# Kernel tuning notes

Measured on AMD Instinct MI355X. Metric: run time of the kernel, lower is better.

## Reference

```python
import jax, jax.numpy as jnp
import numpy as np

B, D, DFF, E, TOPK = 16384, 512, 2048, 8, 2


def setup_inputs() -> dict:
    key = jax.random.key(0)
    ks = jax.random.split(key, 5)
    scale_g = 1.0 / np.sqrt(D)
    scale_1 = 1.0 / np.sqrt(D)
    scale_2 = 1.0 / np.sqrt(DFF)
    return {
        "x": jax.random.normal(ks[0], (B, D), dtype=jnp.float32),
        "Wg": jax.random.normal(ks[1], (D, E), dtype=jnp.float32) * scale_g,
        "W1": jax.random.normal(ks[2], (E, D, DFF), dtype=jnp.float32) * scale_1,
        "b1": jnp.zeros((E, DFF), dtype=jnp.float32),
        "W2": jax.random.normal(ks[3], (E, DFF, D), dtype=jnp.float32) * scale_2,
        "b2": jnp.zeros((E, D), dtype=jnp.float32),
    }


def reference(x, Wg, W1, b1, W2, b2):
    # --- gate: top-k softmax routing weights, zeros elsewhere ---
    logits = x @ Wg                              # [B, E]
    probs = jax.nn.softmax(logits, axis=-1)      # [B, E]
    vals, idx = jax.lax.top_k(probs, TOPK)       # [B, K], [B, K]
    routing = jnp.zeros_like(probs).at[jnp.arange(x.shape[0])[:, None], idx].set(vals)  # [B, E]

    # --- experts: dense FFN per expert (equivalent math to masked dispatch) ---
    # original: gather selected tokens per expert, compute, scatter into
    # zeros[E, B, D], multiply by routing.T[:, :, None], sum over experts.
    # routing weight is exactly 0 for unselected tokens, so the dense form
    # out = sum_e routing[b, e] * expert_e(x_b) computes identical results.
    h = jax.nn.relu(jnp.einsum('bd,edf->ebf', x, W1) + b1[:, None, :])  # [E, B, DFF]
    y = jnp.einsum('ebf,efd->ebd', h, W2) + b2[:, None, :]              # [E, B, D]
    out = jnp.einsum('ebd,be->bd', y, routing)                          # [B, D]
    return out
```

## Files before the change

### kernel.cpp

```cpp
#include <hip/hip_runtime.h>
#include <stdint.h>

#define BTOK 16384
#define DM   512
#define DFF  2048
#define NE   8
#define NPAIR (BTOK*2)
#define MAXT 288

typedef short s16x8 __attribute__((ext_vector_type(8)));
typedef float f32x4 __attribute__((ext_vector_type(4)));

__device__ __forceinline__ uint16_t f2b(float f) {
  uint32_t u = __float_as_uint(f);
  u += 0x7fff + ((u >> 16) & 1);
  return (uint16_t)(u >> 16);
}

__device__ __forceinline__ void g2l16(const void* gp, void* lp) {
  __builtin_amdgcn_global_load_lds(
      (__attribute__((address_space(1))) void*)(void*)gp,
      (__attribute__((address_space(3))) void*)lp, 16, 0, 0);
}

__global__ void k_tr(const float* __restrict__ w1, const float* __restrict__ w2,
                     uint16_t* __restrict__ w1t, uint16_t* __restrict__ w2t) {
  __shared__ float t[32][33];
  int z = blockIdx.z, bx = blockIdx.x;
  int R, C, c0, r0;
  const float* src;
  uint16_t* dst;
  if (z < 8) { R = DM; C = DFF; c0 = (bx & 63) * 32; r0 = (bx >> 6) * 32;
               src = w1 + (size_t)z * R * C; dst = w1t + (size_t)z * R * C; }
  else       { R = DFF; C = DM; c0 = (bx & 15) * 32; r0 = (bx >> 4) * 32;
               src = w2 + (size_t)(z - 8) * R * C; dst = w2t + (size_t)(z - 8) * R * C; }
  int tx = threadIdx.x, ty = threadIdx.y;
#pragma unroll
  for (int j = 0; j < 4; j++)
    t[ty + j * 8][tx] = src[(size_t)(r0 + ty + j * 8) * C + c0 + tx];
  __syncthreads();
#pragma unroll
  for (int j = 0; j < 4; j++)
    dst[(size_t)(c0 + ty + j * 8) * R + r0 + tx] = f2b(t[tx][ty + j * 8]);
}

__global__ __launch_bounds__(256) void k_route(const float* __restrict__ x,
                                               const float* __restrict__ wg,
                                               int* __restrict__ counts,
                                               int* __restrict__ tk_e, float* __restrict__ tk_w,
                                               uint16_t* __restrict__ xb) {
  __shared__ int hist[NE];
  int tid = threadIdx.x, lane = tid & 63, wave = tid >> 6;
  if (tid < NE) hist[tid] = 0;
  __syncthreads();

  float wv[8][8];
#pragma unroll
  for (int j = 0; j < 8; j++) {
    const float4* wr = (const float4*)(wg + (size_t)(j * 64 + lane) * NE);
    float4 a = wr[0], b = wr[1];
    wv[j][0] = a.x; wv[j][1] = a.y; wv[j][2] = a.z; wv[j][3] = a.w;
    wv[j][4] = b.x; wv[j][5] = b.y; wv[j][6] = b.z; wv[j][7] = b.w;
  }

  int tok0 = blockIdx.x * 64 + wave * 16;
  for (int tt = 0; tt < 16; tt++) {
    int tok = tok0 + tt;
    const float* xr = x + (size_t)tok * DM;
    float xv[8];
#pragma unroll
    for (int j = 0; j < 8; j++) xv[j] = xr[j * 64 + lane];
    float acc[NE];
#pragma unroll
    for (int e = 0; e < NE; e++) acc[e] = 0.f;
#pragma unroll
    for (int j = 0; j < 8; j++)
#pragma unroll
      for (int e = 0; e < NE; e++) acc[e] += xv[j] * wv[j][e];
#pragma unroll
    for (int e = 0; e < NE; e++) {
#pragma unroll
      for (int off = 32; off > 0; off >>= 1) acc[e] += __shfl_xor(acc[e], off, 64);
    }
    if (lane == 0) {
      float mx = acc[0];
      for (int e = 1; e < NE; e++) mx = fmaxf(mx, acc[e]);
      float p[NE], s = 0.f;
      for (int e = 0; e < NE; e++) { p[e] = __expf(acc[e] - mx); s += p[e]; }
      float inv = 1.f / s;
      int e0 = 0; float v0 = p[0];
      for (int e = 1; e < NE; e++) if (p[e] > v0) { v0 = p[e]; e0 = e; }
      int e1 = -1; float v1 = -1.f;
      for (int e = 0; e < NE; e++) if (e != e0 && p[e] > v1) { v1 = p[e]; e1 = e; }
      tk_e[tok * 2]     = e0; tk_w[tok * 2]     = v0 * inv;
      tk_e[tok * 2 + 1] = e1; tk_w[tok * 2 + 1] = v1 * inv;
      atomicAdd(&hist[e0], 1);
      atomicAdd(&hist[e1], 1);
    }
  }
  const float* xs = x + (size_t)blockIdx.x * 32768;
  uint16_t* xd = xb + (size_t)blockIdx.x * 32768;
#pragma unroll
  for (int i = 0; i < 16; i++) {
    int o = i * 2048 + tid * 8;
    float4 a = *(const float4*)(xs + o);
    float4 b = *(const float4*)(xs + o + 4);
    uint16_t v[8] = {f2b(a.x), f2b(a.y), f2b(a.z), f2b(a.w),
                     f2b(b.x), f2b(b.y), f2b(b.z), f2b(b.w)};
    *(s16x8*)(xd + o) = *(s16x8*)v;
  }
  __syncthreads();
  if (tid < NE) atomicAdd(&counts[tid], hist[tid]);
}

__global__ void k_setup(const int* __restrict__ counts, int* __restrict__ offsets,
                        int* __restrict__ trB, int* __restrict__ texp, int* __restrict__ ntB) {
  if (threadIdx.x != 0 || blockIdx.x != 0) return;
  int off = 0;
  for (int e = 0; e < NE; e++) { offsets[e] = off; off += counts[e]; }
  offsets[NE] = off;
  int nt = 0;
  for (int e = 0; e < NE; e++)
    for (int r = offsets[e]; r < offsets[e + 1]; r += 128) { trB[nt] = r; texp[nt] = e; nt++; }
  *ntB = nt;
}

__global__ __launch_bounds__(256) void k_build(const int* __restrict__ tk_e, const float* __restrict__ tk_w,
                                               const int* __restrict__ offsets, int* __restrict__ cursors,
                                               int* __restrict__ tok_of, float* __restrict__ w_of,
                                               int* __restrict__ inv) {
  __shared__ int lcnt[NE], lbase[NE];
  int tid = threadIdx.x;
  int i = blockIdx.x * 256 + tid;
  if (tid < NE) lcnt[tid] = 0;
  __syncthreads();
  int e = tk_e[i];
  int local = atomicAdd(&lcnt[e], 1);
  __syncthreads();
  if (tid < NE) lbase[tid] = atomicAdd(&cursors[tid], lcnt[tid]);
  __syncthreads();
  int slot = offsets[e] + lbase[e] + local;
  tok_of[slot] = i >> 1;
  w_of[slot] = tk_w[i];
  inv[i] = slot;
}


#define LDS16(off) (*(const s16x8*)((const char*)smem + (off)))
#define VM6 asm volatile("s_waitcnt vmcnt(6)" ::: "memory")
#define VM0 asm volatile("s_waitcnt vmcnt(0)" ::: "memory")
#define NOVM do{}while(0)
#define NOSTG do{}while(0)
#define MFMA16 __builtin_amdgcn_mfma_f32_16x16x32_bf16
#define BSTR 24576

#define DS0_P(bb) do{ \
  bf0 = LDS16(offB0 + (bb)*BSTR); bf1 = LDS16(offB1 + (bb)*BSTR); \
  bf2 = LDS16(offB2 + (bb)*BSTR); bf3 = LDS16(offB3 + (bb)*BSTR); \
  bf4 = LDS16(offB4 + (bb)*BSTR); bf5 = LDS16(offB5 + (bb)*BSTR); \
  bf6 = LDS16(offB6 + (bb)*BSTR); bf7 = LDS16(offB7 + (bb)*BSTR); \
  af0 = LDS16(offA0 + (bb)*BSTR); af1 = LDS16(offA1 + (bb)*BSTR); }while(0)
#define DS1_P(bb) do{ \
  af2 = LDS16(offA2 + (bb)*BSTR); af3 = LDS16(offA3 + (bb)*BSTR); }while(0)
#define SA_P(bb) do{ \
  g2l16(gA0, (char*)smem + (bb)*BSTR + wave*1024); \
  g2l16(gA1, (char*)smem + (bb)*BSTR + 4096 + wave*1024); \
  gA0 += 32; gA1 += 32; }while(0)
#define SB_P(bb) do{ \
  g2l16(gB0, (char*)smem + (bb)*BSTR + 8192 + wave*1024); \
  g2l16(gB1, (char*)smem + (bb)*BSTR + 12288 + wave*1024); \
  g2l16(gB2, (char*)smem + (bb)*BSTR + 16384 + wave*1024); \
  g2l16(gB3, (char*)smem + (bb)*BSTR + 20480 + wave*1024); \
  gB0 += 32; gB1 += 32; gB2 += 32; gB3 += 32; }while(0)
#define MM16A do{ \
  __builtin_amdgcn_s_setprio(1); \
  acc[0][0] = MFMA16(af0, bf0, acc[0][0], 0, 0, 0); \
  acc[1][0] = MFMA16(af1, bf0, acc[1][0], 0, 0, 0); \
  acc[0][1] = MFMA16(af0, bf1, acc[0][1], 0, 0, 0); \
  acc[1][1] = MFMA16(af1, bf1, acc[1][1], 0, 0, 0); \
  acc[0][2] = MFMA16(af0, bf2, acc[0][2], 0, 0, 0); \
  acc[1][2] = MFMA16(af1, bf2, acc[1][2], 0, 0, 0); \
  acc[0][3] = MFMA16(af0, bf3, acc[0][3], 0, 0, 0); \
  acc[1][3] = MFMA16(af1, bf3, acc[1][3], 0, 0, 0); \
  acc[0][4] = MFMA16(af0, bf4, acc[0][4], 0, 0, 0); \
  acc[1][4] = MFMA16(af1, bf4, acc[1][4], 0, 0, 0); \
  acc[0][5] = MFMA16(af0, bf5, acc[0][5], 0, 0, 0); \
  acc[1][5] = MFMA16(af1, bf5, acc[1][5], 0, 0, 0); \
  acc[0][6] = MFMA16(af0, bf6, acc[0][6], 0, 0, 0); \
  acc[1][6] = MFMA16(af1, bf6, acc[1][6], 0, 0, 0); \
  acc[0][7] = MFMA16(af0, bf7, acc[0][7], 0, 0, 0); \
  acc[1][7] = MFMA16(af1, bf7, acc[1][7], 0, 0, 0); \
  __builtin_amdgcn_s_setprio(0); }while(0)
#define MM16B do{ \
  __builtin_amdgcn_s_setprio(1); \
  acc[2][0] = MFMA16(af2, bf0, acc[2][0], 0, 0, 0); \
  acc[3][0] = MFMA16(af3, bf0, acc[3][0], 0, 0, 0); \
  acc[2][1] = MFMA16(af2, bf1, acc[2][1], 0, 0, 0); \
  acc[3][1] = MFMA16(af3, bf1, acc[3][1], 0, 0, 0); \
  acc[2][2] = MFMA16(af2, bf2, acc[2][2], 0, 0, 0); \
  acc[3][2] = MFMA16(af3, bf2, acc[3][2], 0, 0, 0); \
  acc[2][3] = MFMA16(af2, bf3, acc[2][3], 0, 0, 0); \
  acc[3][3] = MFMA16(af3, bf3, acc[3][3], 0, 0, 0); \
  acc[2][4] = MFMA16(af2, bf4, acc[2][4], 0, 0, 0); \
  acc[3][4] = MFMA16(af3, bf4, acc[3][4], 0, 0, 0); \
  acc[2][5] = MFMA16(af2, bf5, acc[2][5], 0, 0, 0); \
  acc[3][5] = MFMA16(af3, bf5, acc[3][5], 0, 0, 0); \
  acc[2][6] = MFMA16(af2, bf6, acc[2][6], 0, 0, 0); \
  acc[3][6] = MFMA16(af3, bf6, acc[3][6], 0, 0, 0); \
  acc[2][7] = MFMA16(af2, bf7, acc[2][7], 0, 0, 0); \
  acc[3][7] = MFMA16(af3, bf7, acc[3][7], 0, 0, 0); \
  __builtin_amdgcn_s_setprio(0); }while(0)
#define TILEP(bb, SA, SB, VMX) do{ \
  DS0_P(bb); SA; \
  __builtin_amdgcn_s_barrier(); \
  asm volatile("s_waitcnt lgkmcnt(0)" ::: "memory"); \
  MM16A; \
  __builtin_amdgcn_s_barrier(); \
  DS1_P(bb); SB; \
  __builtin_amdgcn_s_barrier(); \
  asm volatile("s_waitcnt lgkmcnt(0)" ::: "memory"); \
  MM16B; \
  VMX; \
  __builtin_amdgcn_s_barrier(); }while(0)

#define GEOM_SETUP \
  int tid = threadIdx.x, lane = tid & 63, wave = tid >> 6; \
  int wm = wave >> 1, wn = wave & 1; \
  int l15 = lane & 15, l4 = lane >> 4; \
  int offA0, offA1, offA2, offA3; \
  int offB0, offB1, offB2, offB3, offB4, offB5, offB6, offB7; \
  { int r; \
    r = wm*64 + 0*16 + l15; offA0 = r*64 + ((l4 ^ ((r>>1)&3)) << 4); \
    r = wm*64 + 1*16 + l15; offA1 = r*64 + ((l4 ^ ((r>>1)&3)) << 4); \
    r = wm*64 + 2*16 + l15; offA2 = r*64 + ((l4 ^ ((r>>1)&3)) << 4); \
    r = wm*64 + 3*16 + l15; offA3 = r*64 + ((l4 ^ ((r>>1)&3)) << 4); \
    r = wn*128 + 0*16 + l15; offB0 = 8192 + r*64 + ((l4 ^ ((r>>1)&3)) << 4); \
    r = wn*128 + 1*16 + l15; offB1 = 8192 + r*64 + ((l4 ^ ((r>>1)&3)) << 4); \
    r = wn*128 + 2*16 + l15; offB2 = 8192 + r*64 + ((l4 ^ ((r>>1)&3)) << 4); \
    r = wn*128 + 3*16 + l15; offB3 = 8192 + r*64 + ((l4 ^ ((r>>1)&3)) << 4); \
    r = wn*128 + 4*16 + l15; offB4 = 8192 + r*64 + ((l4 ^ ((r>>1)&3)) << 4); \
    r = wn*128 + 5*16 + l15; offB5 = 8192 + r*64 + ((l4 ^ ((r>>1)&3)) << 4); \
    r = wn*128 + 6*16 + l15; offB6 = 8192 + r*64 + ((l4 ^ ((r>>1)&3)) << 4); \
    r = wn*128 + 7*16 + l15; offB7 = 8192 + r*64 + ((l4 ^ ((r>>1)&3)) << 4); \
  } \
  int rp = tid >> 2, cp = (tid & 3) ^ ((rp >> 1) & 3);

#define ACC_INIT \
  f32x4 acc[4][8]; \
  _Pragma("unroll") for (int m = 0; m < 4; m++) \
  _Pragma("unroll") for (int n = 0; n < 8; n++) \
  _Pragma("unroll") for (int i = 0; i < 4; i++) acc[m][n][i] = 0.f; \
  s16x8 af0, af1, af2, af3, bf0, bf1, bf2, bf3, bf4, bf5, bf6, bf7;

__global__ __launch_bounds__(256, 2) void k_gemm1(
    const uint16_t* __restrict__ xb, const uint16_t* __restrict__ w1t,
    const float* __restrict__ b1,
    const int* __restrict__ tok_of, const int* __restrict__ offsets,
    const int* __restrict__ trB, const int* __restrict__ texp, const int* __restrict__ ntB,
    uint16_t* __restrict__ h) {
  __shared__ __align__(16) uint16_t smem[36864];
  int id = blockIdx.x;
  int tile = id >> 3, n0 = (id & 7) * 256;
  if (tile >= *ntB) return;
  int e = texp[tile], row0 = trB[tile], end = offsets[e + 1];
  GEOM_SETUP;

  const uint16_t *gA0, *gA1, *gB0, *gB1, *gB2, *gB3;
  { int s0 = row0 + rp;      if (s0 >= end) s0 = end - 1;
    int s1 = row0 + rp + 64; if (s1 >= end) s1 = end - 1;
    gA0 = xb + (size_t)tok_of[s0] * DM + cp * 8;
    gA1 = xb + (size_t)tok_of[s1] * DM + cp * 8; }
  { const uint16_t* wb = w1t + (size_t)e * DFF * DM;
    gB0 = wb + (size_t)(n0 + rp +   0) * DM + cp * 8;
    gB1 = wb + (size_t)(n0 + rp +  64) * DM + cp * 8;
    gB2 = wb + (size_t)(n0 + rp + 128) * DM + cp * 8;
    gB3 = wb + (size_t)(n0 + rp + 192) * DM + cp * 8; }

  ACC_INIT;

  SA_P(0); SB_P(0); SA_P(1); SB_P(1);
  VM6;
  __builtin_amdgcn_s_barrier();

#pragma unroll 1
  for (int g = 0; g < 4; ++g) {
    TILEP(0, SA_P(2), SB_P(2), VM6);
    TILEP(1, SA_P(0), SB_P(0), VM6);
    TILEP(2, SA_P(1), SB_P(1), VM6);
  }
  TILEP(0, SA_P(2), SB_P(2), VM6);
  TILEP(1, SA_P(0), SB_P(0), VM6);
  TILEP(2, NOSTG, NOSTG, VM0);
  TILEP(0, NOSTG, NOSTG, NOVM);

  {
    float bv[8];
#pragma unroll
    for (int n = 0; n < 8; n++) bv[n] = b1[(size_t)e * DFF + n0 + wn * 128 + n * 16 + l15];
    char* wrg = (char*)smem + wave * 4608;
    int rr = lane >> 2, cb = lane & 3;
#pragma unroll
    for (int m = 0; m < 4; m++) {
#pragma unroll
      for (int n = 0; n < 8; n++)
#pragma unroll
        for (int i = 0; i < 4; i++) {
          float v = fmaxf(acc[m][n][i] + bv[n], 0.f);
          *(uint16_t*)(wrg + (l4 * 4 + i) * 272 + (n * 16 + l15) * 2) = f2b(v);
        }
      int gr = row0 + wm * 64 + m * 16 + rr;
      const char* src = wrg + rr * 272 + cb * 64;
      if (gr < end) {
        uint16_t* dst = h + (size_t)gr * DFF + n0 + wn * 128 + cb * 32;
        *(s16x8*)(dst +  0) = *(const s16x8*)(src +  0);
        *(s16x8*)(dst +  8) = *(const s16x8*)(src + 16);
        *(s16x8*)(dst + 16) = *(const s16x8*)(src + 32);
        *(s16x8*)(dst + 24) = *(const s16x8*)(src + 48);
      }
    }
  }
}

__global__ __launch_bounds__(256, 2) void k_gemm2(
    const uint16_t* __restrict__ h, const uint16_t* __restrict__ w2t,
    const float* __restrict__ b2, const float* __restrict__ w_of,
    const int* __restrict__ offsets,
    const int* __restrict__ trB, const int* __restrict__ texp, const int* __restrict__ ntB,
    float* __restrict__ y32) {
  __shared__ __align__(16) uint16_t smem[36864];
  int id = blockIdx.x;
  int tile = id >> 1, n0 = (id & 1) * 256;
  if (tile >= *ntB) return;
  int e = texp[tile], row0 = trB[tile], end = offsets[e + 1];
  GEOM_SETUP;

  const uint16_t *gA0, *gA1, *gB0, *gB1, *gB2, *gB3;
  { int s0 = row0 + rp;      if (s0 >= end) s0 = end - 1;
    int s1 = row0 + rp + 64; if (s1 >= end) s1 = end - 1;
    gA0 = h + (size_t)s0 * DFF + cp * 8;
    gA1 = h + (size_t)s1 * DFF + cp * 8; }
  { const uint16_t* wb = w2t + (size_t)e * DM * DFF;
    gB0 = wb + (size_t)(n0 + rp +   0) * DFF + cp * 8;
    gB1 = wb + (size_t)(n0 + rp +  64) * DFF + cp * 8;
    gB2 = wb + (size_t)(n0 + rp + 128) * DFF + cp * 8;
    gB3 = wb + (size_t)(n0 + rp + 192) * DFF + cp * 8; }

  ACC_INIT;

  SA_P(0); SB_P(0); SA_P(1); SB_P(1);
  VM6;
  __builtin_amdgcn_s_barrier();

#pragma unroll 1
  for (int g = 0; g < 20; ++g) {
    TILEP(0, SA_P(2), SB_P(2), VM6);
    TILEP(1, SA_P(0), SB_P(0), VM6);
    TILEP(2, SA_P(1), SB_P(1), VM6);
  }
  TILEP(0, SA_P(2), SB_P(2), VM6);
  TILEP(1, SA_P(0), SB_P(0), VM6);
  TILEP(2, NOSTG, NOSTG, VM0);
  TILEP(0, NOSTG, NOSTG, NOVM);

  {
    float bv[8];
#pragma unroll
    for (int n = 0; n < 8; n++) bv[n] = b2[(size_t)e * DM + n0 + wn * 128 + n * 16 + l15];
#pragma unroll
    for (int m = 0; m < 4; m++)
#pragma unroll
      for (int i = 0; i < 4; i++) {
        int slot = row0 + wm * 64 + m * 16 + l4 * 4 + i;
        if (slot < end) {
          float wgt = w_of[slot];
          size_t base = (size_t)slot * DM + n0 + wn * 128 + l15;
#pragma unroll
          for (int n = 0; n < 8; n++) y32[base + n * 16] = wgt * (acc[m][n][i] + bv[n]);
        }
      }
  }
}

__global__ __launch_bounds__(256) void k_combine(const float* __restrict__ y32,
                                                 const int* __restrict__ inv,
                                                 float* __restrict__ out) {
  int tid = threadIdx.x;
  int tok = blockIdx.x * 2 + (tid >> 7);
  int c4 = (tid & 127) * 4;
  int s0 = inv[tok * 2], s1 = inv[tok * 2 + 1];
  const float4 a = *(const float4*)(y32 + (size_t)s0 * DM + c4);
  const float4 b = *(const float4*)(y32 + (size_t)s1 * DM + c4);
  *(float4*)(out + (size_t)tok * DM + c4) = make_float4(a.x + b.x, a.y + b.y, a.z + b.z, a.w + b.w);
}

extern "C" void kernel_launch(void* const* d_in, const int* in_sizes, int n_in,
                              void* d_out, int out_size, void* d_ws, size_t ws_size,
                              hipStream_t stream) {
  const float* x  = (const float*)d_in[0];
  const float* wg = (const float*)d_in[1];
  const float* w1 = (const float*)d_in[2];
  const float* b1 = (const float*)d_in[3];
  const float* w2 = (const float*)d_in[4];
  const float* b2 = (const float*)d_in[5];
  float* out = (float*)d_out;

  char* ws = (char*)d_ws;
  const size_t MB = 1024 * 1024;
  uint16_t* xb   = (uint16_t*)ws;
  uint16_t* w1t  = (uint16_t*)(ws + 16 * MB);
  uint16_t* w2t  = (uint16_t*)(ws + 32 * MB);
  uint16_t* hbuf = (uint16_t*)(ws + 48 * MB);
  int* ctrl = (int*)(ws + 176 * MB);
  int*   counts  = ctrl;
  int*   cursors = ctrl + 8;
  int*   offsets = ctrl + 16;
  int*   ntB     = ctrl + 32;
  int*   trB     = ctrl + 64;
  int*   texp    = ctrl + 384;
  int*   tk_e    = ctrl + 1024;
  float* tk_w    = (float*)(ctrl + 1024 + 32768);
  int*   tok_of  = ctrl + 1024 + 2 * 32768;
  float* w_of    = (float*)(ctrl + 1024 + 3 * 32768);
  int*   inv     = ctrl + 1024 + 4 * 32768;
  float* y32     = (float*)(ws + 177 * MB);

  hipMemsetAsync(counts, 0, 16 * sizeof(int), stream);

  k_route<<<BTOK / 64, 256, 0, stream>>>(x, wg, counts, tk_e, tk_w, xb);
  k_tr<<<dim3(1024, 1, 16), dim3(32, 8), 0, stream>>>(w1, w2, w1t, w2t);
  k_setup<<<1, 64, 0, stream>>>(counts, offsets, trB, texp, ntB);
  k_build<<<NPAIR / 256, 256, 0, stream>>>(tk_e, tk_w, offsets, cursors, tok_of, w_of, inv);
  k_gemm1<<<MAXT * 8, 256, 0, stream>>>(xb, w1t, b1, tok_of, offsets,
                                        trB, texp, ntB, hbuf);
  k_gemm2<<<MAXT * 2, 256, 0, stream>>>(hbuf, w2t, b2, w_of, offsets,
                                        trB, texp, ntB, y32);
  k_combine<<<BTOK / 2, 256, 0, stream>>>(y32, inv, out);
}
```

Before: 391.7 us.

## Fuse combine into gemm2 via atomics, remap tiles per XCD, vectorize transpose stores

The separate combine kernel and the fp32 per-slot y32 buffer are removed. gemm2 now atomically adds weighted expert outputs straight into a zeroed output, which saves a full write and read of y32 but costs atomic traffic and a memset. The block-to-tile mapping in both GEMMs is interleaved so blocks with the same id mod 8 (likely one XCD) work on contiguous tiles for better L2 reuse. The weight transpose now writes 16-byte vectors, and setup fills the tile table in parallel.

```diff
diff --git a/kernel.cpp b/kernel.cpp
--- a/kernel.cpp
+++ b/kernel.cpp
@@ -7,6 +7,7 @@
 #define NE   8
 #define NPAIR (BTOK*2)
 #define MAXT 288
+#define TPXMAX 36
 
 typedef short s16x8 __attribute__((ext_vector_type(8)));
 typedef float f32x4 __attribute__((ext_vector_type(4)));
@@ -39,9 +40,14 @@
   for (int j = 0; j < 4; j++)
     t[ty + j * 8][tx] = src[(size_t)(r0 + ty + j * 8) * C + c0 + tx];
   __syncthreads();
-#pragma unroll
-  for (int j = 0; j < 4; j++)
-    dst[(size_t)(c0 + ty + j * 8) * R + r0 + tx] = f2b(t[tx][ty + j * 8]);
+  int tid = ty * 32 + tx;
+  int oc = tid >> 3, ch = tid & 7;
+  if (ch < 4) {
+    uint16_t v[8];
+#pragma unroll
+    for (int k = 0; k < 8; k++) v[k] = f2b(t[ch * 8 + k][oc]);
+    *(s16x8*)(dst + (size_t)(c0 + oc) * R + r0 + ch * 8) = *(s16x8*)v;
+  }
 }
 
 __global__ __launch_bounds__(256) void k_route(const float* __restrict__ x,
@@ -115,20 +121,27 @@
 
 __global__ void k_setup(const int* __restrict__ counts, int* __restrict__ offsets,
                         int* __restrict__ trB, int* __restrict__ texp, int* __restrict__ ntB) {
-  if (threadIdx.x != 0 || blockIdx.x != 0) return;
-  int off = 0;
-  for (int e = 0; e < NE; e++) { offsets[e] = off; off += counts[e]; }
-  offsets[NE] = off;
-  int nt = 0;
-  for (int e = 0; e < NE; e++)
-    for (int r = offsets[e]; r < offsets[e + 1]; r += 128) { trB[nt] = r; texp[nt] = e; nt++; }
-  *ntB = nt;
+  __shared__ int soff[NE + 1], ts[NE + 1];
+  int tid = threadIdx.x;
+  if (tid == 0) {
+    int off = 0;
+    for (int e = 0; e < NE; e++) { soff[e] = off; offsets[e] = off; off += counts[e]; }
+    soff[NE] = off; offsets[NE] = off;
+    int nt = 0;
+    for (int e = 0; e < NE; e++) { ts[e] = nt; nt += (counts[e] + 127) >> 7; }
+    ts[NE] = nt; *ntB = nt;
+  }
+  __syncthreads();
+  if (tid < NE) {
+    int e = tid, base = ts[e], o = soff[e];
+    int n = ts[e + 1] - ts[e];
+    for (int i = 0; i < n; i++) { trB[base + i] = o + i * 128; texp[base + i] = e; }
+  }
 }
 
 __global__ __launch_bounds__(256) void k_build(const int* __restrict__ tk_e, const float* __restrict__ tk_w,
                                                const int* __restrict__ offsets, int* __restrict__ cursors,
-                                               int* __restrict__ tok_of, float* __restrict__ w_of,
-                                               int* __restrict__ inv) {
+                                               int* __restrict__ tok_of, float* __restrict__ w_of) {
   __shared__ int lcnt[NE], lbase[NE];
   int tid = threadIdx.x;
   int i = blockIdx.x * 256 + tid;
@@ -142,7 +155,6 @@
   int slot = offsets[e] + lbase[e] + local;
   tok_of[slot] = i >> 1;
   w_of[slot] = tk_w[i];
-  inv[i] = slot;
 }
 
 
@@ -260,8 +272,12 @@
     uint16_t* __restrict__ h) {
   __shared__ __align__(16) uint16_t smem[36864];
   int id = blockIdx.x;
-  int tile = id >> 3, n0 = (id & 7) * 256;
-  if (tile >= *ntB) return;
+  int nt = *ntB, tpx = (nt + 7) >> 3;
+  int x = id & 7, q = id >> 3, j = q >> 3;
+  if (j >= tpx) return;
+  int tile = x * tpx + j;
+  if (tile >= nt) return;
+  int n0 = (q & 7) * 256;
   int e = texp[tile], row0 = trB[tile], end = offsets[e + 1];
   GEOM_SETUP;
 
@@ -324,13 +340,17 @@
 __global__ __launch_bounds__(256, 2) void k_gemm2(
     const uint16_t* __restrict__ h, const uint16_t* __restrict__ w2t,
     const float* __restrict__ b2, const float* __restrict__ w_of,
-    const int* __restrict__ offsets,
+    const int* __restrict__ tok_of, const int* __restrict__ offsets,
     const int* __restrict__ trB, const int* __restrict__ texp, const int* __restrict__ ntB,
-    float* __restrict__ y32) {
+    float* __restrict__ out) {
   __shared__ __align__(16) uint16_t smem[36864];
   int id = blockIdx.x;
-  int tile = id >> 1, n0 = (id & 1) * 256;
-  if (tile >= *ntB) return;
+  int nt = *ntB, tpx = (nt + 7) >> 3;
+  int x = id & 7, q = id >> 3, j = q >> 1;
+  if (j >= tpx) return;
+  int tile = x * tpx + j;
+  if (tile >= nt) return;
+  int n0 = (q & 1) * 256;
   int e = texp[tile], row0 = trB[tile], end = offsets[e + 1];
   GEOM_SETUP;
 
@@ -373,24 +393,13 @@
         int slot = row0 + wm * 64 + m * 16 + l4 * 4 + i;
         if (slot < end) {
           float wgt = w_of[slot];
-          size_t base = (size_t)slot * DM + n0 + wn * 128 + l15;
-#pragma unroll
-          for (int n = 0; n < 8; n++) y32[base + n * 16] = wgt * (acc[m][n][i] + bv[n]);
+          int tok = tok_of[slot];
+          float* ob = out + (size_t)tok * DM + n0 + wn * 128 + l15;
+#pragma unroll
+          for (int n = 0; n < 8; n++) atomicAdd(ob + n * 16, wgt * (acc[m][n][i] + bv[n]));
         }
       }
   }
-}
-
-__global__ __launch_bounds__(256) void k_combine(const float* __restrict__ y32,
-                                                 const int* __restrict__ inv,
-                                                 float* __restrict__ out) {
-  int tid = threadIdx.x;
-  int tok = blockIdx.x * 2 + (tid >> 7);
-  int c4 = (tid & 127) * 4;
-  int s0 = inv[tok * 2], s1 = inv[tok * 2 + 1];
-  const float4 a = *(const float4*)(y32 + (size_t)s0 * DM + c4);
-  const float4 b = *(const float4*)(y32 + (size_t)s1 * DM + c4);
-  *(float4*)(out + (size_t)tok * DM + c4) = make_float4(a.x + b.x, a.y + b.y, a.z + b.z, a.w + b.w);
 }
 
 extern "C" void kernel_launch(void* const* d_in, const int* in_sizes, int n_in,
@@ -421,18 +430,16 @@
   float* tk_w    = (float*)(ctrl + 1024 + 32768);
   int*   tok_of  = ctrl + 1024 + 2 * 32768;
   float* w_of    = (float*)(ctrl + 1024 + 3 * 32768);
-  int*   inv     = ctrl + 1024 + 4 * 32768;
-  float* y32     = (float*)(ws + 177 * MB);
 
   hipMemsetAsync(counts, 0, 16 * sizeof(int), stream);
+  hipMemsetAsync(d_out, 0, out_size, stream);
 
   k_route<<<BTOK / 64, 256, 0, stream>>>(x, wg, counts, tk_e, tk_w, xb);
   k_tr<<<dim3(1024, 1, 16), dim3(32, 8), 0, stream>>>(w1, w2, w1t, w2t);
   k_setup<<<1, 64, 0, stream>>>(counts, offsets, trB, texp, ntB);
-  k_build<<<NPAIR / 256, 256, 0, stream>>>(tk_e, tk_w, offsets, cursors, tok_of, w_of, inv);
-  k_gemm1<<<MAXT * 8, 256, 0, stream>>>(xb, w1t, b1, tok_of, offsets,
-                                        trB, texp, ntB, hbuf);
-  k_gemm2<<<MAXT * 2, 256, 0, stream>>>(hbuf, w2t, b2, w_of, offsets,
-                                        trB, texp, ntB, y32);
-  k_combine<<<BTOK / 2, 256, 0, stream>>>(y32, inv, out);
-}
+  k_build<<<NPAIR / 256, 256, 0, stream>>>(tk_e, tk_w, offsets, cursors, tok_of, w_of);
+  k_gemm1<<<8 * TPXMAX * 8, 256, 0, stream>>>(xb, w1t, b1, tok_of, offsets,
+                                              trB, texp, ntB, hbuf);
+  k_gemm2<<<8 * TPXMAX * 2, 256, 0, stream>>>(hbuf, w2t, b2, w_of, tok_of, offsets,
+                                              trB, texp, ntB, out);
+}
```

New measurement: 403.2 us. 2.9% more time.
